# Optimization experiments

Measured on AMD Instinct MI355X. Metric: run time of the kernel, lower is better.

Reference implementation:

```python
import jax, jax.numpy as jnp
import numpy as np

E = 256
H = 512
LN_EPS = 1e-5
NORM_EPS = 1e-12


def setup_inputs() -> dict:
    key = jax.random.key(0)
    ks = jax.random.split(key, 8)
    B, N, M = 8, 128, 128
    track_features = jax.random.normal(ks[0], (B, N, E), dtype=jnp.float32)
    det_features = jax.random.normal(ks[1], (B, M, E), dtype=jnp.float32)
    # MLP params (torch Linear default init style: uniform, but values irrelevant for correctness harness)
    lim1 = 1.0 / np.sqrt(3 * E)
    W1 = jax.random.uniform(ks[2], (3 * E, H), minval=-lim1, maxval=lim1, dtype=jnp.float32)
    b1 = jax.random.uniform(ks[3], (H,), minval=-lim1, maxval=lim1, dtype=jnp.float32)
    gamma = jnp.ones((H,), dtype=jnp.float32)
    beta = jnp.zeros((H,), dtype=jnp.float32)
    lim2 = 1.0 / np.sqrt(H)
    W2 = jax.random.uniform(ks[4], (H, 1), minval=-lim2, maxval=lim2, dtype=jnp.float32)
    b2 = jax.random.uniform(ks[5], (1,), minval=-lim2, maxval=lim2, dtype=jnp.float32)
    return {"track_features": track_features, "det_features": det_features,
            "W1": W1, "b1": b1, "gamma": gamma, "beta": beta, "W2": W2, "b2": b2}


def _l2_normalize(x):
    # F.normalize(x, dim=-1): x / max(||x||_2, eps)
    n = jnp.sqrt(jnp.sum(x * x, axis=-1, keepdims=True))
    return x / jnp.maximum(n, NORM_EPS)


def reference(track_features, det_features, W1, b1, gamma, beta, W2, b2):
    t = _l2_normalize(track_features)   # (B, N, E)
    d = _l2_normalize(det_features)     # (B, M, E)
    tb = t[:, :, None, :]               # (B, N, 1, E)
    db = d[:, None, :, :]               # (B, 1, M, E)
    B, N, _ = t.shape
    M = d.shape[1]
    diff = jnp.abs(tb - db)                                  # (B, N, M, E)
    pair = jnp.concatenate([jnp.broadcast_to(tb, (B, N, M, E)),
                            jnp.broadcast_to(db, (B, N, M, E)),
                            diff], axis=-1)                  # (B, N, M, 3E)
    h = jnp.einsum('bnme,eh->bnmh', pair, W1) + b1           # (B, N, M, H)
    mu = jnp.mean(h, axis=-1, keepdims=True)
    var = jnp.mean((h - mu) ** 2, axis=-1, keepdims=True)
    h = (h - mu) * jax.lax.rsqrt(var + LN_EPS) * gamma + beta
    h = h * jax.nn.sigmoid(h)                                # SiLU
    out = jnp.einsum('bnmh,ho->bnmo', h, W2)[..., 0] + b2[0]  # (B, N, M)
    return out
```

## Files before the change

### kernel.cpp

```cpp
#include <hip/hip_runtime.h>
#include <hip/hip_bf16.h>
#include <cstdint>

typedef __bf16 bf16x8 __attribute__((ext_vector_type(8)));
typedef __bf16 bf16x2 __attribute__((ext_vector_type(2)));
typedef float f32x4 __attribute__((ext_vector_type(4)));

#define E_DIM 256
#define H_DIM 512
#define TSTR 260

static __device__ __forceinline__ unsigned pkbf(float a, float b) {
    bf16x2 h;
    h[0] = (__bf16)a;
    h[1] = (__bf16)b;
    return __builtin_bit_cast(unsigned, h);
}

__global__ __launch_bounds__(256)
void w1conv_kernel(const float* __restrict__ W1, __bf16* __restrict__ W1cc) {
    int u = blockIdx.x * 256 + threadIdx.x;
    int j   = u & 3;
    int h   = (u >> 2) & 511;
    int c   = (u >> 11) & 7;
    int mat = u >> 14;
    const float* src = W1 + (size_t)(mat * 256 + c * 32 + j * 8) * H_DIM + h;
    uint4 v;
    v.x = pkbf(src[0], src[(size_t)1 * H_DIM]);
    v.y = pkbf(src[(size_t)2 * H_DIM], src[(size_t)3 * H_DIM]);
    v.z = pkbf(src[(size_t)4 * H_DIM], src[(size_t)5 * H_DIM]);
    v.w = pkbf(src[(size_t)6 * H_DIM], src[(size_t)7 * H_DIM]);
    *(uint4*)(W1cc + ((size_t)(mat * 8 + c) * 512 + h) * 32 + j * 8) = v;
}

__global__ __launch_bounds__(512, 4)
void pq_mfma_kernel(const float* __restrict__ track, const float* __restrict__ det,
                    const __bf16* __restrict__ W1cc, const float* __restrict__ b1,
                    float* __restrict__ P, float* __restrict__ Q) {
    __shared__ __align__(16) __bf16 Ash[32 * 256];
    __shared__ float sclS[32];

    int tid  = threadIdx.x;
    int lane = tid & 63;
    int wave = tid >> 6;
    int lq   = lane >> 4;
    int lc   = lane & 15;

    int blk  = blockIdx.x;
    int mat  = blk >> 6;
    int rowg = (blk >> 1) & 31;
    int half = blk & 1;
    int r0   = rowg * 32;
    int h0   = half * 256;
    const float* src = mat ? det : track;

#pragma unroll
    for (int i = 0; i < 4; ++i) {
        int row = wave * 4 + i;
        float4 x = ((const float4*)(src + (size_t)(r0 + row) * E_DIM))[lane];
        float ss = x.x*x.x + x.y*x.y + x.z*x.z + x.w*x.w;
#pragma unroll
        for (int off = 32; off > 0; off >>= 1) ss += __shfl_xor(ss, off);
        if (lane == 0) sclS[row] = 1.0f / fmaxf(sqrtf(ss), 1e-12f);
    }
    __syncthreads();

#pragma unroll
    for (int r = 0; r < 2; ++r) {
        int row = r * 16 + lc;
        float st = sclS[row];
        const float* gp = src + (size_t)(r0 + row) * E_DIM + wave * 32 + lq * 8;
        float4 t0 = *(const float4*)gp;
        float4 t1 = *(const float4*)(gp + 4);
        uint4 v;
        v.x = pkbf(t0.x * st, t0.y * st);
        v.y = pkbf(t0.z * st, t0.w * st);
        v.z = pkbf(t1.x * st, t1.y * st);
        v.w = pkbf(t1.z * st, t1.w * st);
        *(uint4*)&Ash[(size_t)(r * 512 + wave * 64 + lane) * 8] = v;
    }
    __syncthreads();

    const uint4* Wg = (const uint4*)W1cc + (mat ? 16384 : 0);
    int hb = h0 + wave * 32 + lc;
    bf16x8 bwA[2], bwB[2];
#pragma unroll
    for (int ht = 0; ht < 2; ++ht)
        bwA[ht] = __builtin_bit_cast(bf16x8, Wg[(hb + ht * 16) * 4 + lq]);

    f32x4 acc[2][2];
#pragma unroll
    for (int pt = 0; pt < 2; ++pt)
#pragma unroll
        for (int ht = 0; ht < 2; ++ht)
            acc[pt][ht] = (f32x4){0.f, 0.f, 0.f, 0.f};

#pragma unroll 2
    for (int c = 0; c < 8; ++c) {
        bf16x8* cur = (c & 1) ? bwB : bwA;
        bf16x8* nxt = (c & 1) ? bwA : bwB;
        int c1 = (c + 1) & 7;
#pragma unroll
        for (int ht = 0; ht < 2; ++ht)
            nxt[ht] = __builtin_bit_cast(bf16x8, Wg[c1 * 2048 + (hb + ht * 16) * 4 + lq]);
#pragma unroll
        for (int pt = 0; pt < 2; ++pt) {
            bf16x8 af = *(const bf16x8*)&Ash[(size_t)((pt * 8 + c) * 64 + lane) * 8];
#pragma unroll
            for (int ht = 0; ht < 2; ++ht)
                acc[pt][ht] = __builtin_amdgcn_mfma_f32_16x16x32_bf16(cur[ht], af, acc[pt][ht], 0, 0, 0);
        }
    }

    float* dst = mat ? Q : P;
#pragma unroll
    for (int ht = 0; ht < 2; ++ht) {
        int h = h0 + wave * 32 + ht * 16 + lq * 4;
        f32x4 bvv = (f32x4){0.f, 0.f, 0.f, 0.f};
        if (!mat) bvv = *(const f32x4*)&b1[h];
#pragma unroll
        for (int pt = 0; pt < 2; ++pt) {
            f32x4 o = acc[pt][ht] + bvv;
            *(f32x4*)&dst[(size_t)(r0 + pt * 16 + lc) * H_DIM + h] = o;
        }
    }
}

__global__ __launch_bounds__(512, 4)
void main_kernel(const float* __restrict__ track, const float* __restrict__ det,
                 const __bf16* __restrict__ W1cc,
                 const float* __restrict__ P, const float* __restrict__ Q,
                 const float* __restrict__ gamma, const float* __restrict__ beta,
                 const float* __restrict__ W2, const float* __restrict__ b2,
                 float* __restrict__ out) {
    __shared__ __align__(16) char SMEM[49408];
    __bf16* Ash  = (__bf16*)SMEM;
    float*  tsl  = (float*)(SMEM + 32768);
    float*  dsl  = (float*)(SMEM + 41088);
    float*  LNr1 = (float*)(SMEM + 32768);
    float*  LNr2 = (float*)(SMEM + 35072);
    float*  Red2 = (float*)(SMEM + 37376);
    float*  MuS  = (float*)(SMEM + 39680);
    float*  RsS  = (float*)(SMEM + 39936);
    __shared__ float sclT[8], sclD[8];

    int tid  = threadIdx.x;
    int lane = tid & 63;
    int wave = tid >> 6;
    int lq   = lane >> 4;
    int lc   = lane & 15;

    int blk = blockIdx.x;
    int b   = blk >> 8;
    int n0  = ((blk >> 4) & 15) * 8;
    int m0  = (blk & 15) * 8;

    float4 tstage = ((const float4*)(track + (size_t)(b * 128 + n0 + wave) * E_DIM))[lane];
    float4 dstage = ((const float4*)(det   + (size_t)(b * 128 + m0 + wave) * E_DIM))[lane];

    const uint4* Wg = (const uint4*)W1cc + 32768;
    int hb = wave * 64 + lc;
    bf16x8 bwA[4], bwB[4];
#pragma unroll
    for (int ht = 0; ht < 4; ++ht)
        bwA[ht] = __builtin_bit_cast(bf16x8, Wg[(hb + ht * 16) * 4 + lq]);

    {
        float a = tstage.x*tstage.x + tstage.y*tstage.y + tstage.z*tstage.z + tstage.w*tstage.w;
        float d = dstage.x*dstage.x + dstage.y*dstage.y + dstage.z*dstage.z + dstage.w*dstage.w;
#pragma unroll
        for (int off = 32; off > 0; off >>= 1) { a += __shfl_xor(a, off); d += __shfl_xor(d, off); }
        if (lane == 0) {
            sclT[wave] = 1.0f / fmaxf(sqrtf(a), 1e-12f);
            sclD[wave] = 1.0f / fmaxf(sqrtf(d), 1e-12f);
        }
    }
    *(float4*)&tsl[wave * TSTR + lane * 4] = tstage;
    *(float4*)&dsl[wave * TSTR + lane * 4] = dstage;
    __syncthreads();

    {
        int k0 = wave * 32 + lq * 8;
        int ml = lane & 7;
        float sd = sclD[ml];
        const float* dr = dsl + ml * TSTR + k0;
        float4 d0 = *(const float4*)dr;
        float4 d1 = *(const float4*)(dr + 4);
#pragma unroll
        for (int r = 0; r < 4; ++r) {
            int nl = r * 2 + (lc >> 3);
            float st = sclT[nl];
            const float* tr = tsl + nl * TSTR + k0;
            float4 t0 = *(const float4*)tr;
            float4 t1 = *(const float4*)(tr + 4);
            uint4 v;
            v.x = pkbf(fabsf(t0.x * st - d0.x * sd), fabsf(t0.y * st - d0.y * sd));
            v.y = pkbf(fabsf(t0.z * st - d0.z * sd), fabsf(t0.w * st - d0.w * sd));
            v.z = pkbf(fabsf(t1.x * st - d1.x * sd), fabsf(t1.y * st - d1.y * sd));
            v.w = pkbf(fabsf(t1.z * st - d1.z * sd), fabsf(t1.w * st - d1.w * sd));
            *(uint4*)&Ash[(size_t)(r * 512 + wave * 64 + lane) * 8] = v;
        }
    }

    const float* Pb = P + (size_t)(b * 128 + n0) * H_DIM;
    const float* Qb = Q + (size_t)(b * 128 + m0) * H_DIM;
    f32x4 acc[4][4];
    {
        f32x4 qv[4];
#pragma unroll
        for (int ht = 0; ht < 4; ++ht)
            qv[ht] = *(const f32x4*)&Qb[(size_t)(lc & 7) * H_DIM + wave * 64 + ht * 16 + lq * 4];
#pragma unroll
        for (int pt = 0; pt < 4; ++pt) {
            int n = pt * 2 + (lc >> 3);
#pragma unroll
            for (int ht = 0; ht < 4; ++ht) {
                f32x4 pv = *(const f32x4*)&Pb[(size_t)n * H_DIM + wave * 64 + ht * 16 + lq * 4];
                acc[pt][ht] = pv + qv[ht];
            }
        }
    }
    __syncthreads();

#pragma unroll 2
    for (int c = 0; c < 8; ++c) {
        bf16x8* cur = (c & 1) ? bwB : bwA;
        bf16x8* nxt = (c & 1) ? bwA : bwB;
        int c1 = (c + 1) & 7;
#pragma unroll
        for (int ht = 0; ht < 4; ++ht)
            nxt[ht] = __builtin_bit_cast(bf16x8, Wg[c1 * 2048 + (hb + ht * 16) * 4 + lq]);
#pragma unroll
        for (int pt = 0; pt < 4; ++pt) {
            bf16x8 af = *(const bf16x8*)&Ash[(size_t)((pt * 8 + c) * 64 + lane) * 8];
#pragma unroll
            for (int ht = 0; ht < 4; ++ht)
                acc[pt][ht] = __builtin_amdgcn_mfma_f32_16x16x32_bf16(cur[ht], af, acc[pt][ht], 0, 0, 0);
        }
    }

#pragma unroll
    for (int pt = 0; pt < 4; ++pt) {
        float s1 = 0.f, s2 = 0.f;
#pragma unroll
        for (int ht = 0; ht < 4; ++ht)
#pragma unroll
            for (int rg = 0; rg < 4; ++rg) {
                float v = acc[pt][ht][rg];
                s1 += v; s2 += v * v;
            }
        s1 += __shfl_xor(s1, 16); s2 += __shfl_xor(s2, 16);
        s1 += __shfl_xor(s1, 32); s2 += __shfl_xor(s2, 32);
        if (lq == 0) {
            LNr1[(pt * 16 + lc) * 9 + wave] = s1;
            LNr2[(pt * 16 + lc) * 9 + wave] = s2;
        }
    }
    __syncthreads();
    if (tid < 64) {
        float S1 = 0.f, S2 = 0.f;
#pragma unroll
        for (int w = 0; w < 8; ++w) { S1 += LNr1[tid * 9 + w]; S2 += LNr2[tid * 9 + w]; }
        float mu = S1 * (1.0f / 512.0f);
        float var = S2 * (1.0f / 512.0f) - mu * mu;
        MuS[tid] = mu;
        RsS[tid] = rsqrtf(var + 1e-5f);
    }
    __syncthreads();

    float mus[4], rss[4];
#pragma unroll
    for (int pt = 0; pt < 4; ++pt) { mus[pt] = MuS[pt * 16 + lc]; rss[pt] = RsS[pt * 16 + lc]; }
    float ca[4] = {0.f, 0.f, 0.f, 0.f};
#pragma unroll
    for (int ht = 0; ht < 4; ++ht) {
        int h = wave * 64 + ht * 16 + lq * 4;
        f32x4 g  = *(const f32x4*)&gamma[h];
        f32x4 bb = *(const f32x4*)&beta[h];
        f32x4 w  = *(const f32x4*)&W2[h];
#pragma unroll
        for (int pt = 0; pt < 4; ++pt) {
#pragma unroll
            for (int rg = 0; rg < 4; ++rg) {
                float x = (acc[pt][ht][rg] - mus[pt]) * rss[pt] * g[rg] + bb[rg];
                float sg = __builtin_amdgcn_rcpf(1.0f + __expf(-x));
                ca[pt] += x * sg * w[rg];
            }
        }
    }
#pragma unroll
    for (int pt = 0; pt < 4; ++pt) {
        float c = ca[pt];
        c += __shfl_xor(c, 16);
        c += __shfl_xor(c, 32);
        if (lq == 0) Red2[(pt * 16 + lc) * 9 + wave] = c;
    }
    __syncthreads();
    if (tid < 64) {
        float o = b2[0];
#pragma unroll
        for (int w = 0; w < 8; ++w) o += Red2[tid * 9 + w];
        int n = n0 + (tid >> 3);
        int m = m0 + (tid & 7);
        out[(size_t)(b * 128 + n) * 128 + m] = o;
    }
}

extern "C" void kernel_launch(void* const* d_in, const int* in_sizes, int n_in,
                              void* d_out, int out_size, void* d_ws, size_t ws_size,
                              hipStream_t stream) {
    const float* track = (const float*)d_in[0];
    const float* det   = (const float*)d_in[1];
    const float* W1    = (const float*)d_in[2];
    const float* b1    = (const float*)d_in[3];
    const float* gamma = (const float*)d_in[4];
    const float* beta  = (const float*)d_in[5];
    const float* W2    = (const float*)d_in[6];
    const float* b2    = (const float*)d_in[7];
    float* out = (float*)d_out;

    char* ws = (char*)d_ws;
    float*  P     = (float*)(ws);
    float*  Q     = (float*)(ws + (2u << 20));
    __bf16* W1cc  = (__bf16*)(ws + (4u << 20));

    w1conv_kernel<<<192, 256, 0, stream>>>(W1, W1cc);
    pq_mfma_kernel<<<128, 512, 0, stream>>>(track, det, W1cc, b1, P, Q);
    main_kernel<<<2048, 512, 0, stream>>>(track, det, W1cc, P, Q, gamma, beta, W2, b2, out);
}
```

Measured before the change: 152.4 us.

## Merge weight conversion and P/Q GEMM into one prep kernel, precompute norms

Combines the W1 bf16 conversion and the per-row P/Q projection into a single prep launch. The P/Q blocks now convert their W1 slice from fp32 on the fly instead of waiting for a separate conversion pass, and they write the inverse row norms to workspace. The main kernel reads those norms and loads track/det rows straight from global memory, so it no longer stages them through shared memory or repeats the norm reduction. Other changes: gamma/beta/W2 are staged in LDS, the final reductions use shuffles instead of a single-wave loop, and prep blocks are smaller (16 rows) to raise parallelism, at the cost of extra strided fp32 W1 reads.

```diff
diff --git a/kernel.cpp b/kernel.cpp
--- a/kernel.cpp
+++ b/kernel.cpp
@@ -8,7 +8,6 @@
 
 #define E_DIM 256
 #define H_DIM 512
-#define TSTR 260
 
 static __device__ __forceinline__ unsigned pkbf(float a, float b) {
     bf16x2 h;
@@ -17,28 +16,132 @@
     return __builtin_bit_cast(unsigned, h);
 }
 
-__global__ __launch_bounds__(256)
-void w1conv_kernel(const float* __restrict__ W1, __bf16* __restrict__ W1cc) {
-    int u = blockIdx.x * 256 + threadIdx.x;
-    int j   = u & 3;
-    int h   = (u >> 2) & 511;
-    int c   = (u >> 11) & 7;
-    int mat = u >> 14;
-    const float* src = W1 + (size_t)(mat * 256 + c * 32 + j * 8) * H_DIM + h;
-    uint4 v;
-    v.x = pkbf(src[0], src[(size_t)1 * H_DIM]);
-    v.y = pkbf(src[(size_t)2 * H_DIM], src[(size_t)3 * H_DIM]);
-    v.z = pkbf(src[(size_t)4 * H_DIM], src[(size_t)5 * H_DIM]);
-    v.w = pkbf(src[(size_t)6 * H_DIM], src[(size_t)7 * H_DIM]);
-    *(uint4*)(W1cc + ((size_t)(mat * 8 + c) * 512 + h) * 32 + j * 8) = v;
+__global__ __launch_bounds__(512, 2)
+void prep_kernel(const float* __restrict__ track, const float* __restrict__ det,
+                 const float* __restrict__ W1, const float* __restrict__ b1,
+                 float* __restrict__ P, float* __restrict__ Q,
+                 __bf16* __restrict__ W1cc, float* __restrict__ sclT,
+                 float* __restrict__ sclD) {
+    __shared__ __align__(16) __bf16 Ash[16 * 256];
+    int tid = threadIdx.x;
+    int blk = blockIdx.x;
+
+    if (blk >= 256) {
+        int u = (blk - 256) * 512 + tid;
+        int j = u & 3;
+        int h = (u >> 2) & 511;
+        int c = u >> 11;
+        const float* src = W1 + (size_t)(512 + c * 32 + j * 8) * H_DIM + h;
+        uint4 v;
+        v.x = pkbf(src[0],                 src[(size_t)1 * H_DIM]);
+        v.y = pkbf(src[(size_t)2 * H_DIM], src[(size_t)3 * H_DIM]);
+        v.z = pkbf(src[(size_t)4 * H_DIM], src[(size_t)5 * H_DIM]);
+        v.w = pkbf(src[(size_t)6 * H_DIM], src[(size_t)7 * H_DIM]);
+        *(uint4*)(W1cc + ((size_t)(c * 512 + h) * 32 + j * 8)) = v;
+        return;
+    }
+
+    int lane = tid & 63;
+    int wave = tid >> 6;
+    int lq   = lane >> 4;
+    int lc   = lane & 15;
+    int l5   = lane & 31;
+
+    int mat  = blk >> 7;
+    int rowg = (blk >> 1) & 63;
+    int half = blk & 1;
+    int r0   = rowg * 16;
+    int h0   = half * 256;
+    const float* src = mat ? det : track;
+
+    {
+        int row = wave * 2 + (lane >> 5);
+        const float* gp = src + (size_t)(r0 + row) * E_DIM + l5 * 8;
+        float4 x0 = *(const float4*)gp;
+        float4 x1 = *(const float4*)(gp + 4);
+        float ss = x0.x*x0.x + x0.y*x0.y + x0.z*x0.z + x0.w*x0.w
+                 + x1.x*x1.x + x1.y*x1.y + x1.z*x1.z + x1.w*x1.w;
+#pragma unroll
+        for (int off = 16; off > 0; off >>= 1) ss += __shfl_xor(ss, off);
+        float st = 1.0f / fmaxf(sqrtf(ss), 1e-12f);
+        if (half == 0 && l5 == 0) (mat ? sclD : sclT)[r0 + row] = st;
+        uint4 v;
+        v.x = pkbf(x0.x * st, x0.y * st);
+        v.y = pkbf(x0.z * st, x0.w * st);
+        v.z = pkbf(x1.x * st, x1.y * st);
+        v.w = pkbf(x1.z * st, x1.w * st);
+        int cc = l5 >> 2, j = l5 & 3;
+        *(uint4*)&Ash[(size_t)(cc * 64 + j * 16 + row) * 8] = v;
+    }
+    __syncthreads();
+
+    int hB = h0 + wave * 32 + lc;
+    const float* wb = W1 + (size_t)(mat * 256) * H_DIM + hB;
+    float wf[2][8];
+#pragma unroll
+    for (int ht = 0; ht < 2; ++ht)
+#pragma unroll
+        for (int i = 0; i < 8; ++i)
+            wf[ht][i] = wb[(size_t)(lq * 8 + i) * H_DIM + ht * 16];
+
+    f32x4 acc[2];
+    acc[0] = (f32x4){0.f, 0.f, 0.f, 0.f};
+    acc[1] = (f32x4){0.f, 0.f, 0.f, 0.f};
+
+#pragma unroll
+    for (int c = 0; c < 8; ++c) {
+        bf16x8 cw[2];
+#pragma unroll
+        for (int ht = 0; ht < 2; ++ht) {
+            uint4 u;
+            u.x = pkbf(wf[ht][0], wf[ht][1]);
+            u.y = pkbf(wf[ht][2], wf[ht][3]);
+            u.z = pkbf(wf[ht][4], wf[ht][5]);
+            u.w = pkbf(wf[ht][6], wf[ht][7]);
+            cw[ht] = __builtin_bit_cast(bf16x8, u);
+        }
+        if (c < 7) {
+            const float* nb = wb + (size_t)((c + 1) * 32 + lq * 8) * H_DIM;
+#pragma unroll
+            for (int ht = 0; ht < 2; ++ht)
+#pragma unroll
+                for (int i = 0; i < 8; ++i)
+                    wf[ht][i] = nb[(size_t)i * H_DIM + ht * 16];
+        }
+        bf16x8 af = *(const bf16x8*)&Ash[(size_t)(c * 64 + lane) * 8];
+#pragma unroll
+        for (int ht = 0; ht < 2; ++ht)
+            acc[ht] = __builtin_amdgcn_mfma_f32_16x16x32_bf16(cw[ht], af, acc[ht], 0, 0, 0);
+    }
+
+    float* dst = mat ? Q : P;
+#pragma unroll
+    for (int ht = 0; ht < 2; ++ht) {
+        int h = h0 + wave * 32 + ht * 16 + lq * 4;
+        f32x4 o = acc[ht];
+        if (!mat) o += *(const f32x4*)&b1[h];
+        *(f32x4*)&dst[(size_t)(r0 + lc) * H_DIM + h] = o;
+    }
 }
 
 __global__ __launch_bounds__(512, 4)
-void pq_mfma_kernel(const float* __restrict__ track, const float* __restrict__ det,
-                    const __bf16* __restrict__ W1cc, const float* __restrict__ b1,
-                    float* __restrict__ P, float* __restrict__ Q) {
-    __shared__ __align__(16) __bf16 Ash[32 * 256];
-    __shared__ float sclS[32];
+void main_kernel(const float* __restrict__ track, const float* __restrict__ det,
+                 const __bf16* __restrict__ W1cc,
+                 const float* __restrict__ P, const float* __restrict__ Q,
+                 const float* __restrict__ sclT, const float* __restrict__ sclD,
+                 const float* __restrict__ gamma, const float* __restrict__ beta,
+                 const float* __restrict__ W2, const float* __restrict__ b2,
+                 float* __restrict__ out) {
+    __shared__ __align__(16) char SMEM[46336];
+    __bf16* Ash  = (__bf16*)SMEM;
+    float*  LNr1 = (float*)(SMEM + 32768);
+    float*  LNr2 = (float*)(SMEM + 35072);
+    float*  Red2 = (float*)(SMEM + 37376);
+    float*  MuS  = (float*)(SMEM + 39680);
+    float*  RsS  = (float*)(SMEM + 39936);
+    float*  Gs   = (float*)(SMEM + 40192);
+    float*  Bs   = (float*)(SMEM + 42240);
+    float*  Ws   = (float*)(SMEM + 44288);
 
     int tid  = threadIdx.x;
     int lane = tid & 63;
@@ -46,170 +149,54 @@
     int lq   = lane >> 4;
     int lc   = lane & 15;
 
-    int blk  = blockIdx.x;
-    int mat  = blk >> 6;
-    int rowg = (blk >> 1) & 31;
-    int half = blk & 1;
-    int r0   = rowg * 32;
-    int h0   = half * 256;
-    const float* src = mat ? det : track;
-
-#pragma unroll
-    for (int i = 0; i < 4; ++i) {
-        int row = wave * 4 + i;
-        float4 x = ((const float4*)(src + (size_t)(r0 + row) * E_DIM))[lane];
-        float ss = x.x*x.x + x.y*x.y + x.z*x.z + x.w*x.w;
-#pragma unroll
-        for (int off = 32; off > 0; off >>= 1) ss += __shfl_xor(ss, off);
-        if (lane == 0) sclS[row] = 1.0f / fmaxf(sqrtf(ss), 1e-12f);
-    }
-    __syncthreads();
-
-#pragma unroll
-    for (int r = 0; r < 2; ++r) {
-        int row = r * 16 + lc;
-        float st = sclS[row];
-        const float* gp = src + (size_t)(r0 + row) * E_DIM + wave * 32 + lq * 8;
-        float4 t0 = *(const float4*)gp;
-        float4 t1 = *(const float4*)(gp + 4);
-        uint4 v;
-        v.x = pkbf(t0.x * st, t0.y * st);
-        v.y = pkbf(t0.z * st, t0.w * st);
-        v.z = pkbf(t1.x * st, t1.y * st);
-        v.w = pkbf(t1.z * st, t1.w * st);
-        *(uint4*)&Ash[(size_t)(r * 512 + wave * 64 + lane) * 8] = v;
-    }
-    __syncthreads();
-
-    const uint4* Wg = (const uint4*)W1cc + (mat ? 16384 : 0);
-    int hb = h0 + wave * 32 + lc;
-    bf16x8 bwA[2], bwB[2];
-#pragma unroll
-    for (int ht = 0; ht < 2; ++ht)
-        bwA[ht] = __builtin_bit_cast(bf16x8, Wg[(hb + ht * 16) * 4 + lq]);
-
-    f32x4 acc[2][2];
-#pragma unroll
-    for (int pt = 0; pt < 2; ++pt)
-#pragma unroll
-        for (int ht = 0; ht < 2; ++ht)
-            acc[pt][ht] = (f32x4){0.f, 0.f, 0.f, 0.f};
-
-#pragma unroll 2
-    for (int c = 0; c < 8; ++c) {
-        bf16x8* cur = (c & 1) ? bwB : bwA;
-        bf16x8* nxt = (c & 1) ? bwA : bwB;
-        int c1 = (c + 1) & 7;
-#pragma unroll
-        for (int ht = 0; ht < 2; ++ht)
-            nxt[ht] = __builtin_bit_cast(bf16x8, Wg[c1 * 2048 + (hb + ht * 16) * 4 + lq]);
-#pragma unroll
-        for (int pt = 0; pt < 2; ++pt) {
-            bf16x8 af = *(const bf16x8*)&Ash[(size_t)((pt * 8 + c) * 64 + lane) * 8];
-#pragma unroll
-            for (int ht = 0; ht < 2; ++ht)
-                acc[pt][ht] = __builtin_amdgcn_mfma_f32_16x16x32_bf16(cur[ht], af, acc[pt][ht], 0, 0, 0);
-        }
-    }
-
-    float* dst = mat ? Q : P;
-#pragma unroll
-    for (int ht = 0; ht < 2; ++ht) {
-        int h = h0 + wave * 32 + ht * 16 + lq * 4;
-        f32x4 bvv = (f32x4){0.f, 0.f, 0.f, 0.f};
-        if (!mat) bvv = *(const f32x4*)&b1[h];
-#pragma unroll
-        for (int pt = 0; pt < 2; ++pt) {
-            f32x4 o = acc[pt][ht] + bvv;
-            *(f32x4*)&dst[(size_t)(r0 + pt * 16 + lc) * H_DIM + h] = o;
-        }
-    }
-}
-
-__global__ __launch_bounds__(512, 4)
-void main_kernel(const float* __restrict__ track, const float* __restrict__ det,
-                 const __bf16* __restrict__ W1cc,
-                 const float* __restrict__ P, const float* __restrict__ Q,
-                 const float* __restrict__ gamma, const float* __restrict__ beta,
-                 const float* __restrict__ W2, const float* __restrict__ b2,
-                 float* __restrict__ out) {
-    __shared__ __align__(16) char SMEM[49408];
-    __bf16* Ash  = (__bf16*)SMEM;
-    float*  tsl  = (float*)(SMEM + 32768);
-    float*  dsl  = (float*)(SMEM + 41088);
-    float*  LNr1 = (float*)(SMEM + 32768);
-    float*  LNr2 = (float*)(SMEM + 35072);
-    float*  Red2 = (float*)(SMEM + 37376);
-    float*  MuS  = (float*)(SMEM + 39680);
-    float*  RsS  = (float*)(SMEM + 39936);
-    __shared__ float sclT[8], sclD[8];
-
-    int tid  = threadIdx.x;
-    int lane = tid & 63;
-    int wave = tid >> 6;
-    int lq   = lane >> 4;
-    int lc   = lane & 15;
-
     int blk = blockIdx.x;
     int b   = blk >> 8;
     int n0  = ((blk >> 4) & 15) * 8;
     int m0  = (blk & 15) * 8;
-
-    float4 tstage = ((const float4*)(track + (size_t)(b * 128 + n0 + wave) * E_DIM))[lane];
-    float4 dstage = ((const float4*)(det   + (size_t)(b * 128 + m0 + wave) * E_DIM))[lane];
-
-    const uint4* Wg = (const uint4*)W1cc + 32768;
+    int gn  = b * 128 + n0;
+    int gm  = b * 128 + m0;
+
+    float b2v = b2[0];
+    Gs[tid] = gamma[tid];
+    Bs[tid] = beta[tid];
+    Ws[tid] = W2[tid];
+
+    const uint4* Wg = (const uint4*)W1cc;
     int hb = wave * 64 + lc;
     bf16x8 bwA[4], bwB[4];
 #pragma unroll
     for (int ht = 0; ht < 4; ++ht)
         bwA[ht] = __builtin_bit_cast(bf16x8, Wg[(hb + ht * 16) * 4 + lq]);
 
-    {
-        float a = tstage.x*tstage.x + tstage.y*tstage.y + tstage.z*tstage.z + tstage.w*tstage.w;
-        float d = dstage.x*dstage.x + dstage.y*dstage.y + dstage.z*dstage.z + dstage.w*dstage.w;
-#pragma unroll
-        for (int off = 32; off > 0; off >>= 1) { a += __shfl_xor(a, off); d += __shfl_xor(d, off); }
-        if (lane == 0) {
-            sclT[wave] = 1.0f / fmaxf(sqrtf(a), 1e-12f);
-            sclD[wave] = 1.0f / fmaxf(sqrtf(d), 1e-12f);
-        }
-    }
-    *(float4*)&tsl[wave * TSTR + lane * 4] = tstage;
-    *(float4*)&dsl[wave * TSTR + lane * 4] = dstage;
-    __syncthreads();
-
-    {
-        int k0 = wave * 32 + lq * 8;
-        int ml = lane & 7;
-        float sd = sclD[ml];
-        const float* dr = dsl + ml * TSTR + k0;
-        float4 d0 = *(const float4*)dr;
-        float4 d1 = *(const float4*)(dr + 4);
-#pragma unroll
-        for (int r = 0; r < 4; ++r) {
-            int nl = r * 2 + (lc >> 3);
-            float st = sclT[nl];
-            const float* tr = tsl + nl * TSTR + k0;
-            float4 t0 = *(const float4*)tr;
-            float4 t1 = *(const float4*)(tr + 4);
-            uint4 v;
-            v.x = pkbf(fabsf(t0.x * st - d0.x * sd), fabsf(t0.y * st - d0.y * sd));
-            v.y = pkbf(fabsf(t0.z * st - d0.z * sd), fabsf(t0.w * st - d0.w * sd));
-            v.z = pkbf(fabsf(t1.x * st - d1.x * sd), fabsf(t1.y * st - d1.y * sd));
-            v.w = pkbf(fabsf(t1.z * st - d1.z * sd), fabsf(t1.w * st - d1.w * sd));
-            *(uint4*)&Ash[(size_t)(r * 512 + wave * 64 + lane) * 8] = v;
-        }
-    }
-
-    const float* Pb = P + (size_t)(b * 128 + n0) * H_DIM;
-    const float* Qb = Q + (size_t)(b * 128 + m0) * H_DIM;
+    int k0 = wave * 32 + lq * 8;
+    int ml = lane & 7;
+    float sd = sclD[gm + ml];
+    const float* dr = det + (size_t)(gm + ml) * E_DIM + k0;
+    float4 d0 = *(const float4*)dr;
+    float4 d1 = *(const float4*)(dr + 4);
+#pragma unroll
+    for (int r = 0; r < 4; ++r) {
+        int nl = r * 2 + (lc >> 3);
+        float st = sclT[gn + nl];
+        const float* tr = track + (size_t)(gn + nl) * E_DIM + k0;
+        float4 t0 = *(const float4*)tr;
+        float4 t1 = *(const float4*)(tr + 4);
+        uint4 v;
+        v.x = pkbf(fabsf(t0.x * st - d0.x * sd), fabsf(t0.y * st - d0.y * sd));
+        v.y = pkbf(fabsf(t0.z * st - d0.z * sd), fabsf(t0.w * st - d0.w * sd));
+        v.z = pkbf(fabsf(t1.x * st - d1.x * sd), fabsf(t1.y * st - d1.y * sd));
+        v.w = pkbf(fabsf(t1.z * st - d1.z * sd), fabsf(t1.w * st - d1.w * sd));
+        *(uint4*)&Ash[(size_t)(r * 512 + wave * 64 + lane) * 8] = v;
+    }
+
+    const float* Pb = P + (size_t)gn * H_DIM;
+    const float* Qb = Q + (size_t)gm * H_DIM;
     f32x4 acc[4][4];
     {
         f32x4 qv[4];
 #pragma unroll
         for (int ht = 0; ht < 4; ++ht)
-            qv[ht] = *(const f32x4*)&Qb[(size_t)(lc & 7) * H_DIM + wave * 64 + ht * 16 + lq * 4];
+            qv[ht] = *(const f32x4*)&Qb[(size_t)ml * H_DIM + wave * 64 + ht * 16 + lq * 4];
 #pragma unroll
         for (int pt = 0; pt < 4; ++pt) {
             int n = pt * 2 + (lc >> 3);
@@ -257,14 +244,19 @@
         }
     }
     __syncthreads();
-    if (tid < 64) {
-        float S1 = 0.f, S2 = 0.f;
-#pragma unroll
-        for (int w = 0; w < 8; ++w) { S1 += LNr1[tid * 9 + w]; S2 += LNr2[tid * 9 + w]; }
-        float mu = S1 * (1.0f / 512.0f);
-        float var = S2 * (1.0f / 512.0f) - mu * mu;
-        MuS[tid] = mu;
-        RsS[tid] = rsqrtf(var + 1e-5f);
+    {
+        int p = tid >> 3, w = tid & 7;
+        float s1 = LNr1[p * 9 + w];
+        float s2 = LNr2[p * 9 + w];
+        s1 += __shfl_xor(s1, 1); s2 += __shfl_xor(s2, 1);
+        s1 += __shfl_xor(s1, 2); s2 += __shfl_xor(s2, 2);
+        s1 += __shfl_xor(s1, 4); s2 += __shfl_xor(s2, 4);
+        if (w == 0) {
+            float mu  = s1 * (1.0f / 512.0f);
+            float var = s2 * (1.0f / 512.0f) - mu * mu;
+            MuS[p] = mu;
+            RsS[p] = rsqrtf(var + 1e-5f);
+        }
     }
     __syncthreads();
 
@@ -275,9 +267,9 @@
 #pragma unroll
     for (int ht = 0; ht < 4; ++ht) {
         int h = wave * 64 + ht * 16 + lq * 4;
-        f32x4 g  = *(const f32x4*)&gamma[h];
-        f32x4 bb = *(const f32x4*)&beta[h];
-        f32x4 w  = *(const f32x4*)&W2[h];
+        f32x4 g  = *(const f32x4*)&Gs[h];
+        f32x4 bb = *(const f32x4*)&Bs[h];
+        f32x4 w  = *(const f32x4*)&Ws[h];
 #pragma unroll
         for (int pt = 0; pt < 4; ++pt) {
 #pragma unroll
@@ -290,19 +282,20 @@
     }
 #pragma unroll
     for (int pt = 0; pt < 4; ++pt) {
-        float c = ca[pt];
-        c += __shfl_xor(c, 16);
-        c += __shfl_xor(c, 32);
-        if (lq == 0) Red2[(pt * 16 + lc) * 9 + wave] = c;
-    }
-    __syncthreads();
-    if (tid < 64) {
-        float o = b2[0];
-#pragma unroll
-        for (int w = 0; w < 8; ++w) o += Red2[tid * 9 + w];
-        int n = n0 + (tid >> 3);
-        int m = m0 + (tid & 7);
-        out[(size_t)(b * 128 + n) * 128 + m] = o;
+        float cg = ca[pt];
+        cg += __shfl_xor(cg, 16);
+        cg += __shfl_xor(cg, 32);
+        if (lq == 0) Red2[(pt * 16 + lc) * 9 + wave] = cg;
+    }
+    __syncthreads();
+    {
+        int p = tid >> 3, w = tid & 7;
+        float cg = Red2[p * 9 + w];
+        cg += __shfl_xor(cg, 1);
+        cg += __shfl_xor(cg, 2);
+        cg += __shfl_xor(cg, 4);
+        if (w == 0)
+            out[(size_t)(gn + (p >> 3)) * 128 + m0 + (p & 7)] = b2v + cg;
     }
 }
 
@@ -320,11 +313,13 @@
     float* out = (float*)d_out;
 
     char* ws = (char*)d_ws;
-    float*  P     = (float*)(ws);
-    float*  Q     = (float*)(ws + (2u << 20));
-    __bf16* W1cc  = (__bf16*)(ws + (4u << 20));
-
-    w1conv_kernel<<<192, 256, 0, stream>>>(W1, W1cc);
-    pq_mfma_kernel<<<128, 512, 0, stream>>>(track, det, W1cc, b1, P, Q);
-    main_kernel<<<2048, 512, 0, stream>>>(track, det, W1cc, P, Q, gamma, beta, W2, b2, out);
+    float*  Pp   = (float*)(ws);
+    float*  Qp   = (float*)(ws + (2u << 20));
+    __bf16* W1cc = (__bf16*)(ws + (4u << 20));
+    float*  sclT = (float*)(ws + (4u << 20) + (256u << 10));
+    float*  sclD = (float*)(ws + (4u << 20) + (264u << 10));
+
+    prep_kernel<<<288, 512, 0, stream>>>(track, det, W1, b1, Pp, Qp, W1cc, sclT, sclD);
+    main_kernel<<<2048, 512, 0, stream>>>(track, det, W1cc, Pp, Qp, sclT, sclD,
+                                          gamma, beta, W2, b2, out);
 }
```

Result: faster. 143.5 us (-5.9%).
